# Kernel tuning notes

Hardware: AMD Instinct MI355X
Metric: run time of the kernel (lower is better)

## Reference

```python
import jax, jax.numpy as jnp
import numpy as np
from jax import lax

EPS = 1e-8
ROUTINGS = 3


def squash(u, axis=-1):
    norm = jnp.linalg.norm(u, axis=axis, keepdims=True)
    scale = norm ** 2 / (1 + norm ** 2) / (norm + EPS)
    return scale * u


def conv2d(x, w, b, stride):
    y = lax.conv_general_dilated(x, w, window_strides=(stride, stride), padding='VALID',
                                 dimension_numbers=('NCHW', 'OIHW', 'NCHW'))
    return y + b[None, :, None, None]


def setup_inputs() -> dict:
    key = jax.random.key(0)
    ks = jax.random.split(key, 6)
    x = jax.random.normal(ks[0], (512, 1, 28, 28), dtype=jnp.float32)
    conv1_w = 0.1 * jax.random.normal(ks[1], (256, 1, 9, 9), dtype=jnp.float32)
    conv1_b = 0.1 * jax.random.normal(ks[2], (256,), dtype=jnp.float32)
    pc_w = 0.01 * jax.random.normal(ks[3], (256, 256, 9, 9), dtype=jnp.float32)
    pc_b = 0.01 * jax.random.normal(ks[4], (256,), dtype=jnp.float32)
    caps_w = 0.01 * jax.random.normal(ks[5], (10, 1152, 16, 8), dtype=jnp.float32)
    return {"x": x, "conv1_w": conv1_w, "conv1_b": conv1_b,
            "pc_w": pc_w, "pc_b": pc_b, "caps_w": caps_w}


def reference(x, conv1_w, conv1_b, pc_w, pc_b, caps_w):
    B = x.shape[0]
    # conv1 + relu: [B,1,28,28] -> [B,256,20,20]
    h = jax.nn.relu(conv2d(x, conv1_w, conv1_b, stride=1))
    # primary capsules: [B,256,20,20] -> [B,256,6,6] -> [B,1152,8], squash
    h = conv2d(h, pc_w, pc_b, stride=2)
    u = squash(h.reshape(B, 1152, 8))
    # votes: weight [O,I,Do,Di] x u [B,I,Di] -> x_hat [B,O,I,Do]
    x_hat = jnp.einsum('oidk,bik->boid', caps_w, u)
    x_hat_det = lax.stop_gradient(x_hat)
    b_logits = jnp.zeros((B, caps_w.shape[0], caps_w.shape[1]), dtype=x_hat.dtype)
    out_caps = None
    for i in range(ROUTINGS):
        c = jax.nn.softmax(b_logits, axis=1)  # softmax over output caps
        if i == ROUTINGS - 1:
            out_caps = squash(jnp.sum(c[..., None] * x_hat, axis=2))  # [B,O,Do]
        else:
            v = squash(jnp.sum(c[..., None] * x_hat_det, axis=2))  # [B,O,Do]
            b_logits = b_logits + jnp.einsum('bod,boid->boi', v, x_hat_det)
    length = jnp.linalg.norm(out_caps, axis=-1)  # [B,O]
    return length
```

## Files before the change

kernel.cpp:

```cpp
#include <hip/hip_runtime.h>
#include <hip/hip_bf16.h>
#include <hip/hip_fp16.h>
#include <math.h>

#define EPS 1e-8f

typedef __attribute__((ext_vector_type(8))) short bf16x8;
typedef __attribute__((ext_vector_type(8))) _Float16 f16x8;
typedef __attribute__((ext_vector_type(4))) float f32x4;
typedef __attribute__((ext_vector_type(16))) float f32x16;

__device__ static inline unsigned short f2bf(float f) {
    __hip_bfloat16 h = __float2bfloat16(f);
    return *reinterpret_cast<unsigned short*>(&h);
}
__device__ static inline unsigned short f2h(float f) {
    __half h = __float2half(f);
    return *reinterpret_cast<unsigned short*>(&h);
}

__device__ static inline void gld_lds16(const void* g, void* l) {
    __builtin_amdgcn_global_load_lds((const __attribute__((address_space(1))) void*)g,
                                     (__attribute__((address_space(3))) void*)l, 16, 0, 0);
}

__device__ static inline void h8tof(uint4 w, float* f) {
    float2 a = __half22float2(*(__half2*)&w.x);
    float2 b = __half22float2(*(__half2*)&w.y);
    float2 c = __half22float2(*(__half2*)&w.z);
    float2 d = __half22float2(*(__half2*)&w.w);
    f[0] = a.x; f[1] = a.y; f[2] = b.x; f[3] = b.y;
    f[4] = c.x; f[5] = c.y; f[6] = d.x; f[7] = d.y;
}

__global__ void k_prep(const float* __restrict__ x, unsigned short* __restrict__ xh,
                       const float* __restrict__ w1, unsigned short* __restrict__ wt1h,
                       const float* __restrict__ cw, __half* __restrict__ cwh) {
    int idx = blockIdx.x * 256 + threadIdx.x;
    if (idx < 401408) {
        xh[idx] = f2h(x[idx]);
    } else if (idx < 401408 + 24576) {
        int j = idx - 401408;
        int n = j / 96, k = j % 96;
        wt1h[j] = (k < 81) ? f2h(w1[n * 81 + k]) : (unsigned short)0;
    } else {
        int j = idx - 401408 - 24576;
        cwh[j] = __float2half(cw[j]);
    }
}

__global__ __launch_bounds__(256) void k_tw2(const float* __restrict__ pw,
                                             unsigned short* __restrict__ wt2t) {
    __shared__ unsigned short lds[20736];
    const int oc = blockIdx.x, t = threadIdx.x;
    const float* src = pw + (size_t)oc * 20736;
#pragma unroll
    for (int it = 0; it < 81; ++it) {
        int j = it * 256 + t;
        lds[j] = f2bf(src[j]);
    }
    __syncthreads();
    unsigned short* dst = wt2t + (size_t)oc * 20736;
#pragma unroll
    for (int it = 0; it < 81; ++it) {
        int j = it * 256 + t;
        int q = j >> 8, ic = j & 255;
        dst[j] = lds[ic * 81 + q];
    }
}

__global__ __launch_bounds__(256) void k_conv1(const unsigned short* __restrict__ xh,
                                               const unsigned short* __restrict__ wt1h,
                                               const float* __restrict__ b1,
                                               unsigned short* __restrict__ h1) {
    __shared__ unsigned short Asm[128 * 104];
    __shared__ unsigned short Bsm[128 * 104];
    const int tid = threadIdx.x;
    const int wave = tid >> 6, lane = tid & 63;
    const int ln15 = lane & 15, quad = lane >> 4;
    const int m0 = blockIdx.x * 128;
    const int n0 = blockIdx.y * 128;
    const int wm = (wave >> 1) * 64, wn = (wave & 1) * 64;

    for (int c = tid; c < 1536; c += 256) {
        int r = c / 12, ch = c % 12;
        uint4 v = *(const uint4*)(wt1h + (size_t)(n0 + r) * 96 + ch * 8);
        *(uint4*)(&Bsm[r * 104 + ch * 8]) = v;
    }
    for (int s = 0; s < 5; ++s) {
        int id = s * 256 + tid;
        if (id < 1152) {
            int m_l = id & 127, kh = id >> 7;
            int m = m0 + m_l;
            int b = m / 400, sp = m % 400;
            int oh = sp / 20, ow = sp % 20;
            const unsigned short* src = xh + b * 784 + (oh + kh) * 28 + ow;
            unsigned short* drow = &Asm[m_l * 104 + kh * 9];
#pragma unroll
            for (int w = 0; w < 9; ++w) drow[w] = src[w];
        }
    }
    for (int z = tid; z < 1920; z += 256) {
        int r = z / 15, kk = 81 + z % 15;
        Asm[r * 104 + kk] = 0;
    }
    __syncthreads();

    f32x4 acc[4][4];
#pragma unroll
    for (int i = 0; i < 4; ++i)
#pragma unroll
        for (int j = 0; j < 4; ++j) acc[i][j] = (f32x4)(0.f);

#pragma unroll
    for (int ks = 0; ks < 3; ++ks) {
        int k0 = (ks * 4 + quad) * 8;
        f16x8 af[4], bfr[4];
#pragma unroll
        for (int i = 0; i < 4; ++i)
            af[i] = *(const f16x8*)&Asm[(wm + i * 16 + ln15) * 104 + k0];
#pragma unroll
        for (int j = 0; j < 4; ++j)
            bfr[j] = *(const f16x8*)&Bsm[(wn + j * 16 + ln15) * 104 + k0];
#pragma unroll
        for (int i = 0; i < 4; ++i)
#pragma unroll
            for (int j = 0; j < 4; ++j)
                acc[i][j] = __builtin_amdgcn_mfma_f32_16x16x32_f16(
                    af[i], bfr[j], acc[i][j], 0, 0, 0);
    }

    float bias[4];
#pragma unroll
    for (int j = 0; j < 4; ++j) bias[j] = b1[n0 + wn + j * 16 + ln15];
#pragma unroll
    for (int i = 0; i < 4; ++i) {
#pragma unroll
        for (int r = 0; r < 4; ++r) {
            int m = m0 + wm + i * 16 + quad * 4 + r;
            unsigned short* dst = h1 + (size_t)m * 256 + n0 + wn;
#pragma unroll
            for (int j = 0; j < 4; ++j) {
                float v = acc[i][j][r] + bias[j];
                dst[j * 16 + ln15] = f2bf(v > 0.f ? v : 0.f);
            }
        }
    }
}

__global__ __launch_bounds__(256) void k_conv2(const unsigned short* __restrict__ h1,
                                               const unsigned short* __restrict__ wt2t,
                                               unsigned short* __restrict__ h2a) {
    __shared__ short Asm[128 * 64];
    __shared__ short Bsm[128 * 64];

    const int tid  = threadIdx.x;
    const int wave = tid >> 6, lane = tid & 63;
    const int ln31 = lane & 31, ln7 = lane & 7, khalf = lane >> 5;
    const int m0 = blockIdx.x * 128;
    const int n0 = blockIdx.y * 128;
    const int zz = blockIdx.z;
    const int kt0 = zz * 54;
    const int wm = (wave >> 1) * 64, wn = (wave & 1) * 64;

    const int rbase = wave * 32 + (lane >> 3);
    const int cswz8 = ((lane & 7) ^ ((lane >> 3) & 7)) * 8;

    size_t aptr[4];
    size_t bptr[4];
#pragma unroll
    for (int s = 0; s < 4; ++s) {
        int r = rbase + s * 8;
        int m = m0 + r;
        int b = m / 36, sp = m % 36;
        int oh = sp / 6, ow = sp % 6;
        aptr[s] = (size_t)((b * 20 + 2 * oh) * 20 + 2 * ow) * 256 + cswz8;
        bptr[s] = (size_t)(n0 + r) * 20736 + cswz8;
    }
    short* alds = &Asm[(wave * 32) * 64 + lane * 8];
    short* blds = &Bsm[(wave * 32) * 64 + lane * 8];

    f32x16 acc[2][2];
#pragma unroll
    for (int i = 0; i < 2; ++i)
#pragma unroll
        for (int j = 0; j < 2; ++j) acc[i][j] = (f32x16)(0.f);

    int q0 = kt0 >> 2;
    int kh = q0 / 9, kw = q0 - kh * 9;
    int pix = (kh * 20 + kw) * 256;

    for (int kt = kt0; kt < kt0 + 54; ++kt) {
        size_t aoff = (size_t)pix + ((kt & 3) << 6);
        size_t boff = (size_t)kt << 6;
#pragma unroll
        for (int s = 0; s < 4; ++s)
            gld_lds16(h1 + aptr[s] + aoff, alds + s * 512);
#pragma unroll
        for (int s = 0; s < 4; ++s)
            gld_lds16(wt2t + bptr[s] + boff, blds + s * 512);
        __syncthreads();
#pragma unroll
        for (int ks = 0; ks < 4; ++ks) {
            int slot = ((ks << 1) + khalf) ^ ln7;
            bf16x8 af[2], bfr[2];
#pragma unroll
            for (int i = 0; i < 2; ++i)
                af[i] = *(const bf16x8*)&Asm[(wm + i * 32 + ln31) * 64 + slot * 8];
#pragma unroll
            for (int j = 0; j < 2; ++j)
                bfr[j] = *(const bf16x8*)&Bsm[(wn + j * 32 + ln31) * 64 + slot * 8];
#pragma unroll
            for (int i = 0; i < 2; ++i)
#pragma unroll
                for (int j = 0; j < 2; ++j)
                    acc[i][j] = __builtin_amdgcn_mfma_f32_32x32x16_bf16(
                        af[i], bfr[j], acc[i][j], 0, 0, 0);
        }
        __syncthreads();
        if ((kt & 3) == 3) {
            if (kw == 8) { kw = 0; ++kh; pix += 12 * 256; }
            else         { ++kw;       pix += 256; }
        }
    }

    unsigned short* zs = h2a + (size_t)zz * 4718592;
#pragma unroll
    for (int i = 0; i < 2; ++i) {
#pragma unroll
        for (int j = 0; j < 2; ++j) {
#pragma unroll
            for (int reg = 0; reg < 16; ++reg) {
                int row = (reg & 3) + 8 * (reg >> 2) + 4 * khalf;
                int m = m0 + wm + i * 32 + row;
                zs[(size_t)m * 256 + n0 + wn + j * 32 + ln31] = f2h(acc[i][j][reg]);
            }
        }
    }
}

__global__ __launch_bounds__(256) void k_squash(const unsigned short* __restrict__ h2a,
                                                const float* __restrict__ pb,
                                                unsigned short* __restrict__ u) {
    __shared__ float tile[36 * 260];
    const int tid = threadIdx.x;
    const int b = blockIdx.x;
    const unsigned short* base = h2a + (size_t)b * 9216;
    for (int idx = tid; idx < 1152; idx += 256) {
        int sp = idx >> 5, c8 = (idx & 31) * 8;
        float v[8];
#pragma unroll
        for (int e = 0; e < 8; ++e) v[e] = pb[c8 + e];
#pragma unroll
        for (int z = 0; z < 6; ++z) {
            uint4 w = *(const uint4*)(base + (size_t)z * 4718592 + sp * 256 + c8);
            float f[8];
            h8tof(w, f);
#pragma unroll
            for (int e = 0; e < 8; ++e) v[e] += f[e];
        }
#pragma unroll
        for (int e = 0; e < 8; ++e) tile[sp * 260 + c8 + e] = v[e];
    }
    __syncthreads();
    for (int i2 = tid; i2 < 1152; i2 += 256) {
        int f0 = i2 * 8;
        float val[8];
        float n2 = 0.f;
#pragma unroll
        for (int e = 0; e < 8; ++e) {
            int f = f0 + e;
            int c = f / 36, sp = f - c * 36;
            val[e] = tile[sp * 260 + c];
            n2 += val[e] * val[e];
        }
        float n = sqrtf(n2);
        float s = n2 / (1.f + n2) / (n + EPS);
        unsigned short o8[8];
#pragma unroll
        for (int e = 0; e < 8; ++e) o8[e] = f2h(val[e] * s);
        *(uint4*)(u + (size_t)b * 9216 + f0) = *(uint4*)o8;
    }
}

__global__ __launch_bounds__(256) void k_xhat(const unsigned short* __restrict__ u,
                                              const __half* __restrict__ cwh,
                                              __half* __restrict__ xhat,
                                              float* __restrict__ s0) {
    __shared__ float part[4][16];
    const int b = blockIdx.x, o = blockIdx.y;
    const int t = threadIdx.x;
    const uint4* ub = (const uint4*)(u + (size_t)b * 9216);
    float s_loc[16];
#pragma unroll
    for (int d = 0; d < 16; ++d) s_loc[d] = 0.f;

    for (int i = t; i < 1152; i += 256) {
        float ui[8];
        h8tof(ub[i], ui);
        const uint4* wp = (const uint4*)(cwh + ((size_t)(o * 1152 + i) << 7));
        unsigned short xv[16];
#pragma unroll
        for (int d = 0; d < 16; ++d) {
            float f[8];
            h8tof(wp[d], f);
            float xh = f[0] * ui[0] + f[1] * ui[1] + f[2] * ui[2] + f[3] * ui[3]
                     + f[4] * ui[4] + f[5] * ui[5] + f[6] * ui[6] + f[7] * ui[7];
            s_loc[d] += xh;
            xv[d] = f2h(xh);
        }
        __half* dst = xhat + ((size_t)((b * 10 + o) * 1152 + i)) * 16;
        *(uint4*)dst       = *(uint4*)xv;
        *(uint4*)(dst + 8) = *(uint4*)(xv + 8);
    }
#pragma unroll
    for (int off = 32; off > 0; off >>= 1)
#pragma unroll
        for (int d = 0; d < 16; ++d) s_loc[d] += __shfl_down(s_loc[d], off, 64);
    if ((t & 63) == 0) {
#pragma unroll
        for (int d = 0; d < 16; ++d) part[t >> 6][d] = s_loc[d];
    }
    __syncthreads();
    if (t < 16)
        s0[(b * 10 + o) * 16 + t] = part[0][t] + part[1][t] + part[2][t] + part[3][t];
}

__global__ __launch_bounds__(640) void k_routing(const __half* __restrict__ xhat,
                                                 const float* __restrict__ s0,
                                                 float* __restrict__ out) {
    __shared__ float dots[10][1152];
    __shared__ float sv[10][16];
    __shared__ float vsum[10][16];
    __shared__ float scale_sh[10];
    const int t = threadIdx.x;
    const int b = blockIdx.x;
    const int o = t >> 6, lane = t & 63;
    const __half* xb = xhat + ((size_t)(b * 10 + o) * 1152) * 16;

    if (t < 160) {
        int oo = t >> 4, d = t & 15;
        sv[oo][d] = 0.1f * s0[(b * 10 + oo) * 16 + d];
    }
    __syncthreads();
    if (t < 10) {
        float n2 = 0.f;
#pragma unroll
        for (int d = 0; d < 16; ++d) n2 += sv[t][d] * sv[t][d];
        float n = sqrtf(n2);
        scale_sh[t] = n2 / (1.f + n2) / (n + EPS);
    }
    __syncthreads();
    if (t < 160) vsum[t >> 4][t & 15] = sv[t >> 4][t & 15] * scale_sh[t >> 4];
    __syncthreads();

    for (int pass = 1; pass <= 2; ++pass) {
        float vs[16];
#pragma unroll
        for (int d = 0; d < 16; ++d) vs[d] = vsum[o][d];
        float s_loc[16];
#pragma unroll
        for (int d = 0; d < 16; ++d) s_loc[d] = 0.f;

        for (int g = 0; g < 6; ++g) {
            uint4 xq[3][2];
#pragma unroll
            for (int j = 0; j < 3; ++j) {
                int i = g * 192 + j * 64 + lane;
                const uint4* p = (const uint4*)(xb + (size_t)i * 16);
                xq[j][0] = p[0];
                xq[j][1] = p[1];
                float f0[8], f1[8];
                h8tof(xq[j][0], f0);
                h8tof(xq[j][1], f1);
                float dd = 0.f;
#pragma unroll
                for (int d = 0; d < 8; ++d) dd += vs[d] * f0[d] + vs[d + 8] * f1[d];
                dots[o][i] = dd;
            }
            __syncthreads();
            if (t < 192) {
                int i = g * 192 + t;
                float dv[10];
#pragma unroll
                for (int oo = 0; oo < 10; ++oo) dv[oo] = dots[oo][i];
                float mx = dv[0];
#pragma unroll
                for (int oo = 1; oo < 10; ++oo) mx = fmaxf(mx, dv[oo]);
                float se = 0.f;
#pragma unroll
                for (int oo = 0; oo < 10; ++oo) { dv[oo] = __expf(dv[oo] - mx); se += dv[oo]; }
                float si = 1.f / se;
#pragma unroll
                for (int oo = 0; oo < 10; ++oo) dots[oo][i] = dv[oo] * si;
            }
            __syncthreads();
#pragma unroll
            for (int j = 0; j < 3; ++j) {
                int i = g * 192 + j * 64 + lane;
                float c = dots[o][i];
                float f0[8], f1[8];
                h8tof(xq[j][0], f0);
                h8tof(xq[j][1], f1);
#pragma unroll
                for (int d = 0; d < 8; ++d) {
                    s_loc[d]     += c * f0[d];
                    s_loc[d + 8] += c * f1[d];
                }
            }
        }
#pragma unroll
        for (int off = 32; off > 0; off >>= 1)
#pragma unroll
            for (int d = 0; d < 16; ++d) s_loc[d] += __shfl_down(s_loc[d], off, 64);
        if (lane == 0) {
#pragma unroll
            for (int d = 0; d < 16; ++d) sv[o][d] = s_loc[d];
        }
        __syncthreads();
        if (pass == 1) {
            if (t < 10) {
                float n2 = 0.f;
#pragma unroll
                for (int d = 0; d < 16; ++d) n2 += sv[t][d] * sv[t][d];
                float n = sqrtf(n2);
                scale_sh[t] = n2 / (1.f + n2) / (n + EPS);
            }
            __syncthreads();
            if (t < 160) {
                int oo = t >> 4, d = t & 15;
                vsum[oo][d] += sv[oo][d] * scale_sh[oo];
            }
            __syncthreads();
        } else {
            if (t < 10) {
                float n2 = 0.f;
#pragma unroll
                for (int d = 0; d < 16; ++d) n2 += sv[t][d] * sv[t][d];
                float n = sqrtf(n2);
                out[b * 10 + t] = (n2 / (1.f + n2)) * (n / (n + EPS));
            }
        }
    }
}

extern "C" void kernel_launch(void* const* d_in, const int* in_sizes, int n_in,
                              void* d_out, int out_size, void* d_ws, size_t ws_size,
                              hipStream_t stream) {
    const float* x  = (const float*)d_in[0];
    const float* w1 = (const float*)d_in[1];
    const float* b1 = (const float*)d_in[2];
    const float* pw = (const float*)d_in[3];
    const float* pb = (const float*)d_in[4];
    const float* cw = (const float*)d_in[5];
    float* out = (float*)d_out;

    char* ws = (char*)d_ws;
    unsigned short* h1   = (unsigned short*)ws;
    unsigned short* h2a  = (unsigned short*)(ws + 104857600);
    unsigned short* wt2t = (unsigned short*)(ws + 161480704);
    __half*         xhat = (__half*)ws;
    unsigned short* u    = (unsigned short*)(ws + 188743680);
    __half*         cwh  = (__half*)(ws + 198180864);
    unsigned short* xh16 = (unsigned short*)(ws + 201129984);
    unsigned short* wt1h = (unsigned short*)(ws + 201932800);
    float*          s0   = (float*)(ws + 201981952);

    k_prep<<<7424, 256, 0, stream>>>(x, xh16, w1, wt1h, cw, cwh);
    k_tw2<<<256, 256, 0, stream>>>(pw, wt2t);
    k_conv1<<<dim3(1600, 2), 256, 0, stream>>>(xh16, wt1h, b1, h1);
    k_conv2<<<dim3(144, 2, 6), 256, 0, stream>>>(h1, wt2t, h2a);
    k_squash<<<512, 256, 0, stream>>>(h2a, pb, u);
    k_xhat<<<dim3(512, 10), 256, 0, stream>>>(u, cwh, xhat, s0);
    k_routing<<<512, 640, 0, stream>>>(xhat, s0, out);
}
```

Measured before the change: 622.6 us.

## Split routing into per-chunk pass kernels with atomic accumulation across input chunks

The single routing kernel, which ran 512 blocks and looped serially over six 192-capsule chunks per pass, is replaced by a k_pass kernel launched on a 512x6 grid. Each block handles one chunk and atomically adds its partial sums into a global accumulator, and small kernels apply squash between passes. The first squash of the initial vote sum moves into the tail of k_xhat, and the accumulators are zeroed in k_prep. This raises parallelism sixfold for the bandwidth-bound routing step, at the cost of extra launches, float atomics, and reading xhat from global memory in each pass.

After: 675.5 us. 8.5% more time.

```diff
diff --git a/kernel.cpp b/kernel.cpp
--- a/kernel.cpp
+++ b/kernel.cpp
@@ -35,17 +35,22 @@
 
 __global__ void k_prep(const float* __restrict__ x, unsigned short* __restrict__ xh,
                        const float* __restrict__ w1, unsigned short* __restrict__ wt1h,
-                       const float* __restrict__ cw, __half* __restrict__ cwh) {
+                       const float* __restrict__ cw, __half* __restrict__ cwh,
+                       float* __restrict__ sA, float* __restrict__ sB) {
     int idx = blockIdx.x * 256 + threadIdx.x;
     if (idx < 401408) {
         xh[idx] = f2h(x[idx]);
-    } else if (idx < 401408 + 24576) {
+    } else if (idx < 425984) {
         int j = idx - 401408;
         int n = j / 96, k = j % 96;
         wt1h[j] = (k < 81) ? f2h(w1[n * 81 + k]) : (unsigned short)0;
-    } else {
-        int j = idx - 401408 - 24576;
+    } else if (idx < 1900544) {
+        int j = idx - 425984;
         cwh[j] = __float2half(cw[j]);
+    } else if (idx < 1982464) {
+        sA[idx - 1900544] = 0.f;
+    } else if (idx < 2064384) {
+        sB[idx - 1982464] = 0.f;
     }
 }
 
@@ -286,7 +291,7 @@
 __global__ __launch_bounds__(256) void k_xhat(const unsigned short* __restrict__ u,
                                               const __half* __restrict__ cwh,
                                               __half* __restrict__ xhat,
-                                              float* __restrict__ s0) {
+                                              float* __restrict__ vsum) {
     __shared__ float part[4][16];
     const int b = blockIdx.x, o = blockIdx.y;
     const int t = threadIdx.x;
@@ -322,125 +327,117 @@
         for (int d = 0; d < 16; ++d) part[t >> 6][d] = s_loc[d];
     }
     __syncthreads();
-    if (t < 16)
-        s0[(b * 10 + o) * 16 + t] = part[0][t] + part[1][t] + part[2][t] + part[3][t];
-}
-
-__global__ __launch_bounds__(640) void k_routing(const __half* __restrict__ xhat,
-                                                 const float* __restrict__ s0,
-                                                 float* __restrict__ out) {
-    __shared__ float dots[10][1152];
-    __shared__ float sv[10][16];
-    __shared__ float vsum[10][16];
-    __shared__ float scale_sh[10];
+    if (t < 16) {
+        float s0 = 0.1f * (part[0][t] + part[1][t] + part[2][t] + part[3][t]);
+        float n2 = s0 * s0;
+        n2 += __shfl_xor(n2, 1, 16);
+        n2 += __shfl_xor(n2, 2, 16);
+        n2 += __shfl_xor(n2, 4, 16);
+        n2 += __shfl_xor(n2, 8, 16);
+        float n = sqrtf(n2);
+        float sc = n2 / (1.f + n2) / (n + EPS);
+        vsum[(b * 10 + o) * 16 + t] = s0 * sc;
+    }
+}
+
+__global__ __launch_bounds__(640) void k_pass(const __half* __restrict__ xhat,
+                                              const float* __restrict__ vsum,
+                                              float* __restrict__ sacc) {
+    __shared__ float dots[10][192];
     const int t = threadIdx.x;
-    const int b = blockIdx.x;
+    const int b = blockIdx.x, ic = blockIdx.y;
     const int o = t >> 6, lane = t & 63;
-    const __half* xb = xhat + ((size_t)(b * 10 + o) * 1152) * 16;
-
-    if (t < 160) {
-        int oo = t >> 4, d = t & 15;
-        sv[oo][d] = 0.1f * s0[(b * 10 + oo) * 16 + d];
-    }
-    __syncthreads();
-    if (t < 10) {
-        float n2 = 0.f;
-#pragma unroll
-        for (int d = 0; d < 16; ++d) n2 += sv[t][d] * sv[t][d];
+    const __half* xb = xhat + ((size_t)((b * 10 + o) * 1152) + ic * 192) * 16;
+
+    float vs[16];
+#pragma unroll
+    for (int d = 0; d < 16; ++d) vs[d] = vsum[(b * 10 + o) * 16 + d];
+
+    uint4 xq[3][2];
+#pragma unroll
+    for (int j = 0; j < 3; ++j) {
+        int i = j * 64 + lane;
+        const uint4* p = (const uint4*)(xb + (size_t)i * 16);
+        xq[j][0] = p[0];
+        xq[j][1] = p[1];
+        float f0[8], f1[8];
+        h8tof(xq[j][0], f0);
+        h8tof(xq[j][1], f1);
+        float dd = 0.f;
+#pragma unroll
+        for (int d = 0; d < 8; ++d) dd += vs[d] * f0[d] + vs[d + 8] * f1[d];
+        dots[o][i] = dd;
+    }
+    __syncthreads();
+    if (t < 192) {
+        float dv[10];
+#pragma unroll
+        for (int oo = 0; oo < 10; ++oo) dv[oo] = dots[oo][t];
+        float mx = dv[0];
+#pragma unroll
+        for (int oo = 1; oo < 10; ++oo) mx = fmaxf(mx, dv[oo]);
+        float se = 0.f;
+#pragma unroll
+        for (int oo = 0; oo < 10; ++oo) { dv[oo] = __expf(dv[oo] - mx); se += dv[oo]; }
+        float si = 1.f / se;
+#pragma unroll
+        for (int oo = 0; oo < 10; ++oo) dots[oo][t] = dv[oo] * si;
+    }
+    __syncthreads();
+    float s_loc[16];
+#pragma unroll
+    for (int d = 0; d < 16; ++d) s_loc[d] = 0.f;
+#pragma unroll
+    for (int j = 0; j < 3; ++j) {
+        float c = dots[o][j * 64 + lane];
+        float f0[8], f1[8];
+        h8tof(xq[j][0], f0);
+        h8tof(xq[j][1], f1);
+#pragma unroll
+        for (int d = 0; d < 8; ++d) {
+            s_loc[d]     += c * f0[d];
+            s_loc[d + 8] += c * f1[d];
+        }
+    }
+#pragma unroll
+    for (int off = 32; off > 0; off >>= 1)
+#pragma unroll
+        for (int d = 0; d < 16; ++d) s_loc[d] += __shfl_down(s_loc[d], off, 64);
+    if (lane == 0) {
+#pragma unroll
+        for (int d = 0; d < 16; ++d)
+            atomicAdd(&sacc[(b * 10 + o) * 16 + d], s_loc[d]);
+    }
+}
+
+__global__ __launch_bounds__(256) void k_v2(const float* __restrict__ sacc,
+                                            float* __restrict__ vsum) {
+    int b = blockIdx.x, t = threadIdx.x;
+    if (t >= 160) return;
+    float v = sacc[b * 160 + t];
+    float n2 = v * v;
+    n2 += __shfl_xor(n2, 1, 16);
+    n2 += __shfl_xor(n2, 2, 16);
+    n2 += __shfl_xor(n2, 4, 16);
+    n2 += __shfl_xor(n2, 8, 16);
+    float n = sqrtf(n2);
+    float sc = n2 / (1.f + n2) / (n + EPS);
+    vsum[b * 160 + t] += v * sc;
+}
+
+__global__ __launch_bounds__(256) void k_final(const float* __restrict__ sacc,
+                                               float* __restrict__ out) {
+    int b = blockIdx.x, t = threadIdx.x;
+    if (t >= 160) return;
+    float v = sacc[b * 160 + t];
+    float n2 = v * v;
+    n2 += __shfl_xor(n2, 1, 16);
+    n2 += __shfl_xor(n2, 2, 16);
+    n2 += __shfl_xor(n2, 4, 16);
+    n2 += __shfl_xor(n2, 8, 16);
+    if ((t & 15) == 0) {
         float n = sqrtf(n2);
-        scale_sh[t] = n2 / (1.f + n2) / (n + EPS);
-    }
-    __syncthreads();
-    if (t < 160) vsum[t >> 4][t & 15] = sv[t >> 4][t & 15] * scale_sh[t >> 4];
-    __syncthreads();
-
-    for (int pass = 1; pass <= 2; ++pass) {
-        float vs[16];
-#pragma unroll
-        for (int d = 0; d < 16; ++d) vs[d] = vsum[o][d];
-        float s_loc[16];
-#pragma unroll
-        for (int d = 0; d < 16; ++d) s_loc[d] = 0.f;
-
-        for (int g = 0; g < 6; ++g) {
-            uint4 xq[3][2];
-#pragma unroll
-            for (int j = 0; j < 3; ++j) {
-                int i = g * 192 + j * 64 + lane;
-                const uint4* p = (const uint4*)(xb + (size_t)i * 16);
-                xq[j][0] = p[0];
-                xq[j][1] = p[1];
-                float f0[8], f1[8];
-                h8tof(xq[j][0], f0);
-                h8tof(xq[j][1], f1);
-                float dd = 0.f;
-#pragma unroll
-                for (int d = 0; d < 8; ++d) dd += vs[d] * f0[d] + vs[d + 8] * f1[d];
-                dots[o][i] = dd;
-            }
-            __syncthreads();
-            if (t < 192) {
-                int i = g * 192 + t;
-                float dv[10];
-#pragma unroll
-                for (int oo = 0; oo < 10; ++oo) dv[oo] = dots[oo][i];
-                float mx = dv[0];
-#pragma unroll
-                for (int oo = 1; oo < 10; ++oo) mx = fmaxf(mx, dv[oo]);
-                float se = 0.f;
-#pragma unroll
-                for (int oo = 0; oo < 10; ++oo) { dv[oo] = __expf(dv[oo] - mx); se += dv[oo]; }
-                float si = 1.f / se;
-#pragma unroll
-                for (int oo = 0; oo < 10; ++oo) dots[oo][i] = dv[oo] * si;
-            }
-            __syncthreads();
-#pragma unroll
-            for (int j = 0; j < 3; ++j) {
-                int i = g * 192 + j * 64 + lane;
-                float c = dots[o][i];
-                float f0[8], f1[8];
-                h8tof(xq[j][0], f0);
-                h8tof(xq[j][1], f1);
-#pragma unroll
-                for (int d = 0; d < 8; ++d) {
-                    s_loc[d]     += c * f0[d];
-                    s_loc[d + 8] += c * f1[d];
-                }
-            }
-        }
-#pragma unroll
-        for (int off = 32; off > 0; off >>= 1)
-#pragma unroll
-            for (int d = 0; d < 16; ++d) s_loc[d] += __shfl_down(s_loc[d], off, 64);
-        if (lane == 0) {
-#pragma unroll
-            for (int d = 0; d < 16; ++d) sv[o][d] = s_loc[d];
-        }
-        __syncthreads();
-        if (pass == 1) {
-            if (t < 10) {
-                float n2 = 0.f;
-#pragma unroll
-                for (int d = 0; d < 16; ++d) n2 += sv[t][d] * sv[t][d];
-                float n = sqrtf(n2);
-                scale_sh[t] = n2 / (1.f + n2) / (n + EPS);
-            }
-            __syncthreads();
-            if (t < 160) {
-                int oo = t >> 4, d = t & 15;
-                vsum[oo][d] += sv[oo][d] * scale_sh[oo];
-            }
-            __syncthreads();
-        } else {
-            if (t < 10) {
-                float n2 = 0.f;
-#pragma unroll
-                for (int d = 0; d < 16; ++d) n2 += sv[t][d] * sv[t][d];
-                float n = sqrtf(n2);
-                out[b * 10 + t] = (n2 / (1.f + n2)) * (n / (n + EPS));
-            }
-        }
+        out[b * 10 + (t >> 4)] = (n2 / (1.f + n2)) * (n / (n + EPS));
     }
 }
 
@@ -464,13 +461,18 @@
     __half*         cwh  = (__half*)(ws + 198180864);
     unsigned short* xh16 = (unsigned short*)(ws + 201129984);
     unsigned short* wt1h = (unsigned short*)(ws + 201932800);
-    float*          s0   = (float*)(ws + 201981952);
-
-    k_prep<<<7424, 256, 0, stream>>>(x, xh16, w1, wt1h, cw, cwh);
+    float*          vsum = (float*)(ws + 201981952);
+    float*          sA   = (float*)(ws + 202309632);
+    float*          sB   = (float*)(ws + 202637312);
+
+    k_prep<<<8064, 256, 0, stream>>>(x, xh16, w1, wt1h, cw, cwh, sA, sB);
     k_tw2<<<256, 256, 0, stream>>>(pw, wt2t);
     k_conv1<<<dim3(1600, 2), 256, 0, stream>>>(xh16, wt1h, b1, h1);
     k_conv2<<<dim3(144, 2, 6), 256, 0, stream>>>(h1, wt2t, h2a);
     k_squash<<<512, 256, 0, stream>>>(h2a, pb, u);
-    k_xhat<<<dim3(512, 10), 256, 0, stream>>>(u, cwh, xhat, s0);
-    k_routing<<<512, 640, 0, stream>>>(xhat, s0, out);
-}
+    k_xhat<<<dim3(512, 10), 256, 0, stream>>>(u, cwh, xhat, vsum);
+    k_pass<<<dim3(512, 6), 640, 0, stream>>>(xhat, vsum, sA);
+    k_v2<<<512, 256, 0, stream>>>(sA, vsum);
+    k_pass<<<dim3(512, 6), 640, 0, stream>>>(xhat, vsum, sB);
+    k_final<<<512, 256, 0, stream>>>(sB, out);
+}
```
